# Performance work log

Hardware: AMD Instinct MI355X
Metric: run time of the kernel (lower is better)

## Reference

```python
import jax, jax.numpy as jnp
import numpy as np

N_NODES = 50000
N_EDGES = 800000
IN_DIM = 256
HID = 64
HEADS = 4
N_CLASSES = 40
NEG_SLOPE = 0.2  # DGL GATConv default LeakyReLU slope


def setup_inputs() -> dict:
    key = jax.random.key(0)
    ks = jax.random.split(key, 8)
    features = jax.random.normal(ks[0], (N_NODES, IN_DIM), dtype=jnp.float32)
    src = jax.random.randint(ks[1], (N_EDGES,), 0, N_NODES, dtype=jnp.int32)
    dst = jax.random.randint(ks[2], (N_EDGES,), 0, N_NODES, dtype=jnp.int32)
    # GATConv params (Xavier-ish scale)
    W0 = jax.random.normal(ks[3], (IN_DIM, HEADS * HID), dtype=jnp.float32) / np.sqrt(IN_DIM)
    attn_l = jax.random.normal(ks[4], (HEADS, HID), dtype=jnp.float32) / np.sqrt(HID)
    attn_r = jax.random.normal(ks[5], (HEADS, HID), dtype=jnp.float32) / np.sqrt(HID)
    # Final FC layer
    fc_W = jax.random.normal(ks[6], (HEADS * HID, N_CLASSES), dtype=jnp.float32) / np.sqrt(HEADS * HID)
    fc_b = jax.random.normal(ks[7], (N_CLASSES,), dtype=jnp.float32) * 0.01
    return {"features": features, "W0": W0, "attn_l": attn_l, "attn_r": attn_r,
            "fc_W": fc_W, "fc_b": fc_b, "src": src, "dst": dst}


def _gat_conv(feat, W, a_l, a_r, src, dst):
    # feat: [N, F_in] -> projected [N, H, D]
    h = (feat @ W).reshape(feat.shape[0], HEADS, HID)
    el = jnp.einsum('nhd,hd->nh', h, a_l)  # [N, H]
    er = jnp.einsum('nhd,hd->nh', h, a_r)  # [N, H]
    e = el[src] + er[dst]                  # [E, H]
    e = jnp.where(e > 0, e, NEG_SLOPE * e)  # LeakyReLU
    # segment softmax over incoming edges of each destination node
    m = jax.ops.segment_max(e, dst, num_segments=N_NODES)  # [N, H]
    m = jnp.where(jnp.isfinite(m), m, 0.0)
    ex = jnp.exp(e - m[dst])
    s = jax.ops.segment_sum(ex, dst, num_segments=N_NODES)  # [N, H]
    alpha = ex / s[dst]                                      # [E, H]
    # weighted aggregation of source features
    msgs = alpha[:, :, None] * h[src]                        # [E, H, D]
    return jax.ops.segment_sum(msgs, dst, num_segments=N_NODES)  # [N, H, D]


def reference(features, W0, attn_l, attn_r, fc_W, fc_b, src, dst):
    h = _gat_conv(features, W0, attn_l, attn_r, src, dst)   # [N, H, D]
    h = jax.nn.relu(h).reshape(N_NODES, HEADS * HID)        # flatten(1)
    # dropout is identity in eval mode (training=False)
    return h @ fc_W + fc_b                                  # [N, num_classes]
```

## Files before the change

### kernel.cpp

```cpp
#include <hip/hip_runtime.h>

#define N_NODES 50000
#define N_EDGES 800000
#define IN_DIM 256
#define HID 64
#define HEADS 4
#define NFEAT 256
#define N_CLASSES 40
#define NC_PAD 48
#define NEG_SLOPE 0.2f
#define BIN_CAP 64

typedef __attribute__((ext_vector_type(8))) short short8;
typedef __attribute__((ext_vector_type(4))) float f32x4;

__device__ __forceinline__ unsigned short f2bf(float x) {
    unsigned u = __float_as_uint(x);
    unsigned r = u + 0x7FFFu + ((u >> 16) & 1u);
    return (unsigned short)(r >> 16);
}
__device__ __forceinline__ float bf2f(unsigned short u) {
    return __uint_as_float(((unsigned)u) << 16);
}
__device__ __forceinline__ float bf_lo(unsigned u) {
    return __uint_as_float(u << 16);
}
__device__ __forceinline__ float bf_hi(unsigned u) {
    return __uint_as_float(u & 0xFFFF0000u);
}

__global__ __launch_bounds__(256) void pack_weights(
    const float* __restrict__ W0, unsigned short* __restrict__ Wf,
    const float* __restrict__ W2, unsigned short* __restrict__ Wf2,
    int* __restrict__ cnt)
{
    int t = blockIdx.x * 256 + threadIdx.x;
    if (t < N_NODES) cnt[t] = 0;
    if (t < 65536) {
        int c = t & 255;
        int k = t >> 8;
        int kb = k >> 5, r = k & 31;
        int g = r >> 3, e = r & 7;
        Wf[((size_t)(kb * 256 + c) * 4 + g) * 8 + e] = f2bf(W0[(size_t)k * 256 + c]);
    } else {
        int t2 = t - 65536;
        if (t2 >= 8 * NC_PAD * 32) return;
        int c = (t2 >> 5) % NC_PAD;
        int kb = t2 / (NC_PAD * 32);
        int r = t2 & 31;
        int g = r >> 3, e = r & 7;
        int k = kb * 32 + g * 8 + e;
        float v = (c < N_CLASSES) ? W2[(size_t)k * N_CLASSES + c] : 0.f;
        Wf2[((size_t)(kb * NC_PAD + c) * 4 + g) * 8 + e] = f2bf(v);
    }
}

__global__ __launch_bounds__(256) void proj_mfma(
    const float* __restrict__ feat, const unsigned short* __restrict__ Wf,
    const float* __restrict__ al, const float* __restrict__ ar,
    unsigned short* __restrict__ hb16, float* __restrict__ el, float* __restrict__ er)
{
    const int tid  = threadIdx.x;
    const int lane = tid & 63;
    const int w    = tid >> 6;
    const int c    = lane & 15;
    const int g    = lane >> 4;
    const int row0 = blockIdx.x * 64;

    float alv[16], arv[16];
    #pragma unroll
    for (int f = 0; f < 16; ++f) { alv[f] = al[f * 16 + c]; arv[f] = ar[f * 16 + c]; }

    f32x4 acc[16];
    #pragma unroll
    for (int f = 0; f < 16; ++f) acc[f] = (f32x4){0.f, 0.f, 0.f, 0.f};

    const int arow = min(row0 + w * 16 + c, N_NODES - 1);
    const float* ap = &feat[(size_t)arow * IN_DIM + g * 8];

    for (int kb = 0; kb < 8; ++kb) {
        float4 v0 = *reinterpret_cast<const float4*>(ap + kb * 32);
        float4 v1 = *reinterpret_cast<const float4*>(ap + kb * 32 + 4);
        unsigned short us[8];
        us[0]=f2bf(v0.x); us[1]=f2bf(v0.y); us[2]=f2bf(v0.z); us[3]=f2bf(v0.w);
        us[4]=f2bf(v1.x); us[5]=f2bf(v1.y); us[6]=f2bf(v1.z); us[7]=f2bf(v1.w);
        short8 av = *reinterpret_cast<short8*>(us);
        #pragma unroll
        for (int f = 0; f < 16; ++f) {
            short8 bv = *reinterpret_cast<const short8*>(
                &Wf[((size_t)(kb * 256 + f * 16 + c) * 4 + g) * 8]);
            acc[f] = __builtin_amdgcn_mfma_f32_16x16x32_bf16(av, bv, acc[f], 0, 0, 0);
        }
    }

    const int baserow = row0 + w * 16 + g * 4;
    #pragma unroll
    for (int reg = 0; reg < 4; ++reg) {
        int grow = baserow + reg;
        bool ok = grow < N_NODES;
        float pl[4] = {0.f,0.f,0.f,0.f}, pr[4] = {0.f,0.f,0.f,0.f};
        #pragma unroll
        for (int f = 0; f < 16; ++f) {
            float v = acc[f][reg];
            pl[f >> 2] += v * alv[f];
            pr[f >> 2] += v * arv[f];
            if (ok) hb16[(size_t)grow * NFEAT + f * 16 + c] = f2bf(v);
        }
        #pragma unroll
        for (int hh = 0; hh < 4; ++hh) {
            #pragma unroll
            for (int off = 8; off; off >>= 1) {
                pl[hh] += __shfl_xor(pl[hh], off);
                pr[hh] += __shfl_xor(pr[hh], off);
            }
        }
        if (ok && c == 0) {
            #pragma unroll
            for (int hh = 0; hh < 4; ++hh) {
                el[grow * 4 + hh] = pl[hh];
                er[grow * 4 + hh] = pr[hh];
            }
        }
    }
}

__global__ __launch_bounds__(256) void fc_mfma(
    const unsigned short* __restrict__ aggb, const unsigned short* __restrict__ Wf2,
    const float* __restrict__ bias, float* __restrict__ out)
{
    const int tid  = threadIdx.x;
    const int lane = tid & 63;
    const int w    = tid >> 6;
    const int c    = lane & 15;
    const int g    = lane >> 4;
    const int row0 = blockIdx.x * 64;

    f32x4 acc[3];
    #pragma unroll
    for (int f = 0; f < 3; ++f) acc[f] = (f32x4){0.f, 0.f, 0.f, 0.f};

    const int arow = min(row0 + w * 16 + c, N_NODES - 1);
    const unsigned short* ap = &aggb[(size_t)arow * NFEAT + g * 8];

    for (int kb = 0; kb < 8; ++kb) {
        short8 av = *reinterpret_cast<const short8*>(ap + kb * 32);
        #pragma unroll
        for (int f = 0; f < 3; ++f) {
            short8 bv = *reinterpret_cast<const short8*>(
                &Wf2[((size_t)(kb * NC_PAD + f * 16 + c) * 4 + g) * 8]);
            acc[f] = __builtin_amdgcn_mfma_f32_16x16x32_bf16(av, bv, acc[f], 0, 0, 0);
        }
    }

    const int baserow = row0 + w * 16 + g * 4;
    #pragma unroll
    for (int reg = 0; reg < 4; ++reg) {
        int grow = baserow + reg;
        if (grow >= N_NODES) continue;
        #pragma unroll
        for (int f = 0; f < 3; ++f) {
            int col = f * 16 + c;
            if (col < N_CLASSES)
                out[(size_t)grow * N_CLASSES + col] = acc[f][reg] + bias[col];
        }
    }
}

__global__ __launch_bounds__(256) void scatter_bins(
    const int* __restrict__ src, const int* __restrict__ dst,
    int* __restrict__ cnt,
    const float4* __restrict__ el4, const float4* __restrict__ er4,
    uint4* __restrict__ bins)
{
    int e = blockIdx.x * 256 + threadIdx.x;
    if (e >= N_EDGES) return;
    int d = dst[e], s = src[e];
    int pos = atomicAdd(&cnt[d], 1);
    if (pos >= BIN_CAP) return;
    float4 l = el4[s];
    float4 r = er4[d];
    float t0 = l.x + r.x; t0 = t0 > 0.f ? t0 : NEG_SLOPE * t0;
    float t1 = l.y + r.y; t1 = t1 > 0.f ? t1 : NEG_SLOPE * t1;
    float t2 = l.z + r.z; t2 = t2 > 0.f ? t2 : NEG_SLOPE * t2;
    float t3 = l.w + r.w; t3 = t3 > 0.f ? t3 : NEG_SLOPE * t3;
    unsigned y = (unsigned)f2bf(__expf(t0)) | ((unsigned)f2bf(__expf(t1)) << 16);
    unsigned z = (unsigned)f2bf(__expf(t2)) | ((unsigned)f2bf(__expf(t3)) << 16);
    bins[(d << 6) + pos] = make_uint4((unsigned)s, y, z, 0u);
}

__global__ __launch_bounds__(256) void gat_agg_kernel(
    const int* __restrict__ cnt, const uint4* __restrict__ bins,
    const uint4* __restrict__ hb4, uint4* __restrict__ aggb4)
{
    const int lane  = threadIdx.x & 63;
    const int w     = threadIdx.x >> 6;
    const int d     = blockIdx.x * 4 + w;
    const int hlane = lane & 31;
    const int head  = hlane >> 3;
    const int ehalf = lane >> 5;
    const bool hi   = (head & 1) != 0;

    if (d >= N_NODES) return;
    const int deg = cnt[d];

    uint4 entry = make_uint4(0u, 0u, 0u, 0u);
    if (lane < deg) entry = bins[(d << 6) + lane];
    const int sreg = (int)entry.x;
    const int wy   = (int)entry.y;
    const int wz   = (int)entry.z;

    float acc[8] = {0.f,0.f,0.f,0.f,0.f,0.f,0.f,0.f};
    float sm = 0.f;
    const uint4* hp = hb4 + hlane;

    #pragma unroll 4
    for (int jj = 0; jj < deg; jj += 2) {
        int idx  = jj + ehalf;
        int bidx = idx << 2;
        int s  = __builtin_amdgcn_ds_bpermute(bidx, sreg);
        int ey = __builtin_amdgcn_ds_bpermute(bidx, wy);
        int ez = __builtin_amdgcn_ds_bpermute(bidx, wz);
        unsigned ew = (head & 2) ? (unsigned)ez : (unsigned)ey;
        float ex = hi ? bf_hi(ew) : bf_lo(ew);
        bool valid = idx < deg;
        ex = valid ? ex : 0.f;
        s  = valid ? s : 0;
        sm += ex;
        uint4 pv = hp[(size_t)((unsigned)s << 5)];
        acc[0] = fmaf(ex, bf_lo(pv.x), acc[0]);
        acc[1] = fmaf(ex, bf_hi(pv.x), acc[1]);
        acc[2] = fmaf(ex, bf_lo(pv.y), acc[2]);
        acc[3] = fmaf(ex, bf_hi(pv.y), acc[3]);
        acc[4] = fmaf(ex, bf_lo(pv.z), acc[4]);
        acc[5] = fmaf(ex, bf_hi(pv.z), acc[5]);
        acc[6] = fmaf(ex, bf_lo(pv.w), acc[6]);
        acc[7] = fmaf(ex, bf_hi(pv.w), acc[7]);
    }

    #pragma unroll
    for (int i = 0; i < 8; ++i) acc[i] += __shfl_xor(acc[i], 32);
    sm += __shfl_xor(sm, 32);

    const float inv = (deg > 0) ? 1.f / sm : 0.f;
    if (ehalf == 0) {
        uint4 r;
        r.x = (unsigned)f2bf(fmaxf(acc[0]*inv, 0.f)) | ((unsigned)f2bf(fmaxf(acc[1]*inv, 0.f)) << 16);
        r.y = (unsigned)f2bf(fmaxf(acc[2]*inv, 0.f)) | ((unsigned)f2bf(fmaxf(acc[3]*inv, 0.f)) << 16);
        r.z = (unsigned)f2bf(fmaxf(acc[4]*inv, 0.f)) | ((unsigned)f2bf(fmaxf(acc[5]*inv, 0.f)) << 16);
        r.w = (unsigned)f2bf(fmaxf(acc[6]*inv, 0.f)) | ((unsigned)f2bf(fmaxf(acc[7]*inv, 0.f)) << 16);
        aggb4[(d << 5) + hlane] = r;
    }
}

extern "C" void kernel_launch(void* const* d_in, const int* in_sizes, int n_in,
                              void* d_out, int out_size, void* d_ws, size_t ws_size,
                              hipStream_t stream)
{
    const float* features = (const float*)d_in[0];
    const float* W0       = (const float*)d_in[1];
    const float* attn_l   = (const float*)d_in[2];
    const float* attn_r   = (const float*)d_in[3];
    const float* fc_W     = (const float*)d_in[4];
    const float* fc_b     = (const float*)d_in[5];
    const int*   src      = (const int*)d_in[6];
    const int*   dst      = (const int*)d_in[7];
    float* out = (float*)d_out;

    char* ws = (char*)d_ws;
    unsigned short* hb16 = (unsigned short*)ws;
    ws += (size_t)N_NODES * NFEAT * sizeof(unsigned short);
    unsigned short* aggb = (unsigned short*)ws;
    ws += (size_t)N_NODES * NFEAT * sizeof(unsigned short);
    unsigned short* Wf = (unsigned short*)ws;
    ws += (size_t)IN_DIM * NFEAT * sizeof(unsigned short);
    unsigned short* Wf2 = (unsigned short*)ws;
    ws += (size_t)8 * NC_PAD * 32 * sizeof(unsigned short);
    float* el = (float*)ws;  ws += (size_t)N_NODES * HEADS * sizeof(float);
    float* er = (float*)ws;  ws += (size_t)N_NODES * HEADS * sizeof(float);
    int* cnt = (int*)ws;     ws += (size_t)N_NODES * sizeof(int);
    ws += (16 - ((size_t)ws & 15)) & 15;
    uint4* bins = (uint4*)ws;

    pack_weights<<<(65536 + 8 * NC_PAD * 32 + 255) / 256, 256, 0, stream>>>(
        W0, Wf, fc_W, Wf2, cnt);

    proj_mfma<<<(N_NODES + 63) / 64, 256, 0, stream>>>(
        features, Wf, attn_l, attn_r, hb16, el, er);

    scatter_bins<<<(N_EDGES + 255) / 256, 256, 0, stream>>>(
        src, dst, cnt, (const float4*)el, (const float4*)er, bins);

    gat_agg_kernel<<<(N_NODES + 3) / 4, 256, 0, stream>>>(
        cnt, bins, (const uint4*)hb16, (uint4*)aggb);

    fc_mfma<<<(N_NODES + 63) / 64, 256, 0, stream>>>(aggb, Wf2, fc_b, out);
}
```

Baseline: 165.9 us.

## Split GAT aggregation into feature slices per block for L2 locality

Restructures the aggregation kernel so each block handles one of eight 32-feature slices for eight destination nodes, with 16 edges processed in parallel per wave and 4 lanes per edge. Each wave now reads bin entries directly instead of using cross-lane permutes, and reduces across edge groups with a shuffle tree. The intent is to shrink the per-block gather footprint so that source-feature rows are reused through cache, and to raise memory-level parallelism for low-degree nodes. The cost is that bin entries are reloaded once per slice and the reduction needs more shuffles.

```diff
diff --git a/kernel.cpp b/kernel.cpp
--- a/kernel.cpp
+++ b/kernel.cpp
@@ -194,61 +194,56 @@
 {
     const int lane  = threadIdx.x & 63;
     const int w     = threadIdx.x >> 6;
-    const int d     = blockIdx.x * 4 + w;
-    const int hlane = lane & 31;
-    const int head  = hlane >> 3;
-    const int ehalf = lane >> 5;
-    const bool hi   = (head & 1) != 0;
-
-    if (d >= N_NODES) return;
-    const int deg = cnt[d];
-
-    uint4 entry = make_uint4(0u, 0u, 0u, 0u);
-    if (lane < deg) entry = bins[(d << 6) + lane];
-    const int sreg = (int)entry.x;
-    const int wy   = (int)entry.y;
-    const int wz   = (int)entry.z;
-
-    float acc[8] = {0.f,0.f,0.f,0.f,0.f,0.f,0.f,0.f};
-    float sm = 0.f;
-    const uint4* hp = hb4 + hlane;
-
-    #pragma unroll 4
-    for (int jj = 0; jj < deg; jj += 2) {
-        int idx  = jj + ehalf;
-        int bidx = idx << 2;
-        int s  = __builtin_amdgcn_ds_bpermute(bidx, sreg);
-        int ey = __builtin_amdgcn_ds_bpermute(bidx, wy);
-        int ez = __builtin_amdgcn_ds_bpermute(bidx, wz);
-        unsigned ew = (head & 2) ? (unsigned)ez : (unsigned)ey;
-        float ex = hi ? bf_hi(ew) : bf_lo(ew);
-        bool valid = idx < deg;
-        ex = valid ? ex : 0.f;
-        s  = valid ? s : 0;
-        sm += ex;
-        uint4 pv = hp[(size_t)((unsigned)s << 5)];
-        acc[0] = fmaf(ex, bf_lo(pv.x), acc[0]);
-        acc[1] = fmaf(ex, bf_hi(pv.x), acc[1]);
-        acc[2] = fmaf(ex, bf_lo(pv.y), acc[2]);
-        acc[3] = fmaf(ex, bf_hi(pv.y), acc[3]);
-        acc[4] = fmaf(ex, bf_lo(pv.z), acc[4]);
-        acc[5] = fmaf(ex, bf_hi(pv.z), acc[5]);
-        acc[6] = fmaf(ex, bf_lo(pv.w), acc[6]);
-        acc[7] = fmaf(ex, bf_hi(pv.w), acc[7]);
-    }
-
-    #pragma unroll
-    for (int i = 0; i < 8; ++i) acc[i] += __shfl_xor(acc[i], 32);
-    sm += __shfl_xor(sm, 32);
-
-    const float inv = (deg > 0) ? 1.f / sm : 0.f;
-    if (ehalf == 0) {
-        uint4 r;
-        r.x = (unsigned)f2bf(fmaxf(acc[0]*inv, 0.f)) | ((unsigned)f2bf(fmaxf(acc[1]*inv, 0.f)) << 16);
-        r.y = (unsigned)f2bf(fmaxf(acc[2]*inv, 0.f)) | ((unsigned)f2bf(fmaxf(acc[3]*inv, 0.f)) << 16);
-        r.z = (unsigned)f2bf(fmaxf(acc[4]*inv, 0.f)) | ((unsigned)f2bf(fmaxf(acc[5]*inv, 0.f)) << 16);
-        r.w = (unsigned)f2bf(fmaxf(acc[6]*inv, 0.f)) | ((unsigned)f2bf(fmaxf(acc[7]*inv, 0.f)) << 16);
-        aggb4[(d << 5) + hlane] = r;
+    const int slice = blockIdx.x & 7;
+    const int ng    = blockIdx.x >> 3;
+    const int head  = slice >> 1;
+    const int eg    = lane >> 2;
+    const int q     = lane & 3;
+    const uint4* hp = hb4 + slice * 4 + q;
+
+    #pragma unroll
+    for (int t = 0; t < 2; ++t) {
+        const int d = ng * 8 + w * 2 + t;
+        const int deg = min(cnt[d], BIN_CAP);
+        float acc[8] = {0.f,0.f,0.f,0.f,0.f,0.f,0.f,0.f};
+        float sm = 0.f;
+
+        for (int jj = 0; jj < deg; jj += 16) {
+            int e = jj + eg;
+            uint4 entry = bins[(d << 6) + min(e, deg - 1)];
+            bool valid = e < deg;
+            unsigned ew = (head & 2) ? entry.z : entry.y;
+            float ex = (head & 1) ? bf_hi(ew) : bf_lo(ew);
+            ex = valid ? ex : 0.f;
+            unsigned s = valid ? entry.x : 0u;
+            sm += ex;
+            uint4 pv = hp[(size_t)s * 32];
+            acc[0] = fmaf(ex, bf_lo(pv.x), acc[0]);
+            acc[1] = fmaf(ex, bf_hi(pv.x), acc[1]);
+            acc[2] = fmaf(ex, bf_lo(pv.y), acc[2]);
+            acc[3] = fmaf(ex, bf_hi(pv.y), acc[3]);
+            acc[4] = fmaf(ex, bf_lo(pv.z), acc[4]);
+            acc[5] = fmaf(ex, bf_hi(pv.z), acc[5]);
+            acc[6] = fmaf(ex, bf_lo(pv.w), acc[6]);
+            acc[7] = fmaf(ex, bf_hi(pv.w), acc[7]);
+        }
+
+        #pragma unroll
+        for (int off = 4; off <= 32; off <<= 1) {
+            sm += __shfl_xor(sm, off);
+            #pragma unroll
+            for (int i = 0; i < 8; ++i) acc[i] += __shfl_xor(acc[i], off);
+        }
+
+        const float inv = (deg > 0) ? 1.f / sm : 0.f;
+        if (eg == 0) {
+            uint4 r;
+            r.x = (unsigned)f2bf(fmaxf(acc[0]*inv, 0.f)) | ((unsigned)f2bf(fmaxf(acc[1]*inv, 0.f)) << 16);
+            r.y = (unsigned)f2bf(fmaxf(acc[2]*inv, 0.f)) | ((unsigned)f2bf(fmaxf(acc[3]*inv, 0.f)) << 16);
+            r.z = (unsigned)f2bf(fmaxf(acc[4]*inv, 0.f)) | ((unsigned)f2bf(fmaxf(acc[5]*inv, 0.f)) << 16);
+            r.w = (unsigned)f2bf(fmaxf(acc[6]*inv, 0.f)) | ((unsigned)f2bf(fmaxf(acc[7]*inv, 0.f)) << 16);
+            aggb4[(d << 5) + slice * 4 + q] = r;
+        }
     }
 }
 
@@ -290,7 +285,7 @@
     scatter_bins<<<(N_EDGES + 255) / 256, 256, 0, stream>>>(
         src, dst, cnt, (const float4*)el, (const float4*)er, bins);
 
-    gat_agg_kernel<<<(N_NODES + 3) / 4, 256, 0, stream>>>(
+    gat_agg_kernel<<<(N_NODES / 8) * 8, 256, 0, stream>>>(
         cnt, bins, (const uint4*)hb16, (uint4*)aggb);
 
     fc_mfma<<<(N_NODES + 63) / 64, 256, 0, stream>>>(aggb, Wf2, fc_b, out);
```

Measured after the change: 259.3 us. 56.3% more time.
